# Performance work log

Measured on AMD Instinct MI355X. Metric: run time of the kernel, lower is better.

## Reference

```python
import jax, jax.numpy as jnp
import numpy as np

SMOOTH = 1.0
P = 2
NUM_ITERS = 200  # kornia connected_components num_iterations


def _maxpool3x3(x):
    # F.max_pool2d(x, kernel_size=3, stride=1, padding=1) equivalent (NCHW)
    return jax.lax.reduce_window(
        x, -jnp.inf, jax.lax.max,
        window_dimensions=(1, 1, 3, 3),
        window_strides=(1, 1, 1, 1),
        padding='SAME',
    )


def connected_components(mask_f, num_iterations=NUM_ITERS):
    # kornia-style iterative label propagation on a (B,1,H,W) binary mask.
    # labels initialized to unique pixel ids where mask==1, 0 elsewhere,
    # then 3x3 max-pool propagated, keeping background pinned at 0.
    B, C, H, W = mask_f.shape
    mask = mask_f > 0
    init = jnp.arange(B * C * H * W, dtype=mask_f.dtype).reshape(B, C, H, W)
    out = jnp.where(mask, init, 0.0)

    def body(i, o):
        return jnp.where(mask, _maxpool3x3(o), 0.0)

    return jax.lax.fori_loop(0, num_iterations, body, out)


def setup_inputs() -> dict:
    key = jax.random.key(0)
    k1, k2 = jax.random.split(key)
    B, H, W = 16, 512, 512
    predict = jax.random.uniform(k1, (B, 1, H, W), dtype=jnp.float32)
    target = jax.random.uniform(k2, (B, 1, H, W), dtype=jnp.float32)
    return {"predict": predict, "target": target}


def reference(predict, target):
    B = predict.shape[0]
    # threshold at half of global max -> binary mask (non-differentiable)
    binmask = (predict > (predict.max() / 2)).astype(predict.dtype)
    labels = connected_components(jax.lax.stop_gradient(binmask))

    # torch.numel(torch.unique(labels)) via sort + adjacent-diff count (jit-safe)
    s = jnp.sort(labels.reshape(-1))
    n_unique = 1 + jnp.sum(s[1:] != s[:-1])

    penalty = n_unique.astype(jnp.float32) / B
    penalty = jnp.where(penalty < 1.0, jnp.float32(B), penalty)
    penalty = jnp.minimum(penalty, jnp.float32(B))

    p = predict.reshape(B, -1)
    t = target.reshape(B, -1)
    num = jnp.sum(p * t, axis=1) + SMOOTH
    den = jnp.sum(p ** P + t ** P, axis=1) + SMOOTH
    loss = 1.0 - num / den
    return loss.mean() * penalty  # reduction='mean'
```

## Files before the change

### kernel.cpp

```cpp
#include <hip/hip_runtime.h>
#include <hip/hip_cooperative_groups.h>
#include <stdint.h>

namespace cg = cooperative_groups;

#define NPIX   (16 * 512 * 512)
#define IMG    (512 * 512)
#define NB     16

#define CORE   64
#define HALO   8
#define KIT    8
#define NROUND 25
#define TW     88
#define TH     82
#define TX0    4

#define BM_WORDS  (NPIX / 32)
#define NREP      16
#define SAT       256u
#define MAX3(a, b, c) max(max((a), (b)), (c))

__global__ __launch_bounds__(256) void k_maxdice(const float4* __restrict__ pr4,
                                                 const float4* __restrict__ tg4,
                                                 unsigned int* __restrict__ umax,
                                                 float* __restrict__ num,
                                                 float* __restrict__ den) {
    unsigned int m = 0;
    float sn = 0.f, sd = 0.f;
    int base = blockIdx.x * 1024;
#pragma unroll
    for (int k = 0; k < 4; ++k) {
        int i4 = base + k * 256 + threadIdx.x;
        float4 p = pr4[i4], t = tg4[i4];
        m = max(m, __float_as_uint(p.x));
        m = max(m, __float_as_uint(p.y));
        m = max(m, __float_as_uint(p.z));
        m = max(m, __float_as_uint(p.w));
        sn += p.x * t.x + p.y * t.y + p.z * t.z + p.w * t.w;
        sd += p.x * p.x + p.y * p.y + p.z * p.z + p.w * p.w
            + t.x * t.x + t.y * t.y + t.z * t.z + t.w * t.w;
    }
    for (int o = 32; o > 0; o >>= 1) {
        m  = max(m, (unsigned int)__shfl_down(m, o, 64));
        sn += __shfl_down(sn, o, 64);
        sd += __shfl_down(sd, o, 64);
    }
    __shared__ unsigned int sm[4];
    __shared__ float wn[4], wd[4];
    int lane = threadIdx.x & 63, w = threadIdx.x >> 6;
    if (lane == 0) { sm[w] = m; wn[w] = sn; wd[w] = sd; }
    __syncthreads();
    if (threadIdx.x == 0) {
        atomicMax(umax, max(max(sm[0], sm[1]), max(sm[2], sm[3])));
        int b = blockIdx.x >> 6;
        atomicAdd(&num[b * 32], wn[0] + wn[1] + wn[2] + wn[3]);
        atomicAdd(&den[b * 32], wd[0] + wd[1] + wd[2] + wd[3]);
    }
}

__global__ __launch_bounds__(256) void k_iso(const float* __restrict__ pr,
                                             const unsigned int* __restrict__ umax,
                                             unsigned int* __restrict__ isoCnt) {
    const float thr = __uint_as_float(*umax) * 0.5f;
    unsigned int cnt = 0;
    const int tid = threadIdx.x;
    for (int k = 0; k < 8; ++k) {
        int i4 = (blockIdx.x * 8 + k) * 256 + tid;
        int px = i4 * 4;
        int y   = (px >> 9) & 511;
        int gxr = px & 511;
        float4 c = *(const float4*)(pr + px);
        bool m0 = c.x > thr, m1 = c.y > thr, m2 = c.z > thr, m3 = c.w > thr;
        bool lc = (gxr > 0)   && pr[px - 1] > thr;
        bool rc = (gxr < 508) && pr[px + 4] > thr;
        bool u0 = false, u1 = false, u2 = false, u3 = false, lu = false, ru = false;
        if (y > 0) {
            float4 u = *(const float4*)(pr + px - 512);
            u0 = u.x > thr; u1 = u.y > thr; u2 = u.z > thr; u3 = u.w > thr;
            lu = (gxr > 0)   && pr[px - 513] > thr;
            ru = (gxr < 508) && pr[px - 508] > thr;
        }
        bool d0 = false, d1 = false, d2 = false, d3 = false, ld = false, rd = false;
        if (y < 511) {
            float4 d = *(const float4*)(pr + px + 512);
            d0 = d.x > thr; d1 = d.y > thr; d2 = d.z > thr; d3 = d.w > thr;
            ld = (gxr > 0)   && pr[px + 511] > thr;
            rd = (gxr < 508) && pr[px + 516] > thr;
        }
        bool v0 = u0 | d0, v1 = u1 | d1, v2 = u2 | d2, v3 = u3 | d3;
        bool cmL = lu | lc | ld, cmR = ru | rc | rd;
        bool cm0 = v0 | m0, cm1 = v1 | m1, cm2 = v2 | m2, cm3 = v3 | m3;
        cnt += (m0 && !(cmL | cm1 | v0) && px > 0) ? 1u : 0u;
        cnt += (m1 && !(cm0 | cm2 | v1)) ? 1u : 0u;
        cnt += (m2 && !(cm1 | cm3 | v2)) ? 1u : 0u;
        cnt += (m3 && !(cm2 | cmR | v3)) ? 1u : 0u;
    }
    for (int o = 32; o > 0; o >>= 1)
        cnt += __shfl_down(cnt, o, 64);
    __shared__ unsigned int sc[4];
    int lane = tid & 63, w = tid >> 6;
    if (lane == 0) sc[w] = cnt;
    __syncthreads();
    if (tid == 0)
        atomicAdd(isoCnt, sc[0] + sc[1] + sc[2] + sc[3]);
}

__global__ __launch_bounds__(256, 4) void k_prop_all(const float* __restrict__ pr,
                                                     int* __restrict__ bufA,
                                                     int* __restrict__ bufB,
                                                     unsigned int* __restrict__ bm,
                                                     const unsigned int* __restrict__ umax,
                                                     const unsigned int* __restrict__ isoCnt) {
    if (*isoCnt >= SAT) return;
    cg::grid_group grid = cg::this_grid();
    __shared__ int T[TH * TW];
    const float thr = __uint_as_float(*umax) * 0.5f;
    const int tid  = threadIdx.x;
    const int blk  = blockIdx.x;
    const int bx   = blk & 7, by = (blk >> 3) & 7, bimg = blk >> 6;
    const int gx0  = bx * CORE - HALO;
    const int gy0  = by * CORE - HALO;
    int* const base0 = bufA + bimg * IMG;
    int* const base1 = bufB + bimg * IMG;
    const float* img = pr + bimg * IMG;

    {
        int4* bmz = (int4*)bm;
        for (int u = blk * 256 + tid; u < NREP * BM_WORDS / 4; u += 1024 * 256)
            bmz[u] = make_int4(0, 0, 0, 0);
    }

    if (tid < TW) { T[tid] = -1; T[81 * TW + tid] = -1; }
    if (tid < 80) { T[(tid + 1) * TW + 3] = -1; T[(tid + 1) * TW + 84] = -1; }
    for (int u = tid; u < 1600; u += 256) {
        int r = u / 20, c = (u % 20) * 4;
        int gy = gy0 + r, gx = gx0 + c;
        int4 v;
        if (gy >= 0 && gy < 512 && gx >= 0 && gx < 512) {
            float4 pv = *(const float4*)(img + (gy << 9) + gx);
            int id = bimg * IMG + (gy << 9) + gx;
            v.x = (pv.x > thr) ? id     : -1;
            v.y = (pv.y > thr) ? id + 1 : -1;
            v.z = (pv.z > thr) ? id + 2 : -1;
            v.w = (pv.w > thr) ? id + 3 : -1;
        } else v = make_int4(-1, -1, -1, -1);
        *(int4*)&T[(r + 1) * TW + TX0 + c] = v;
    }
    __syncthreads();
    grid.sync();

    const bool active = (tid < 200);
    const int cu = tid % 20, ru = tid / 20;
    const int x0 = cu * 4;
    const int yr = ru * 8;
    int4 O[8];

#define LOAD_ROW(y, V, VL, VR) do {                            \
        const int* _r = &T[((y) + 1) * TW + TX0 + x0];         \
        V  = *(const int4*)_r;                                 \
        VL = _r[-1];                                           \
        VR = _r[4];                                            \
    } while (0)

    for (int r = 0; r < NROUND; ++r) {
        for (int it = 0; it < KIT; ++it) {
            if (active) {
                int4 A, B, C; int Al, Ar, Bl, Br, Cl, Cr;
                LOAD_ROW(yr - 1, A, Al, Ar);
                LOAD_ROW(yr,     B, Bl, Br);
#pragma unroll
                for (int j = 0; j < 8; ++j) {
                    LOAD_ROW(yr + j + 1, C, Cl, Cr);
                    int4 col;
                    col.x = MAX3(A.x, B.x, C.x);
                    col.y = MAX3(A.y, B.y, C.y);
                    col.z = MAX3(A.z, B.z, C.z);
                    col.w = MAX3(A.w, B.w, C.w);
                    int cl = MAX3(Al, Bl, Cl);
                    int cr = MAX3(Ar, Br, Cr);
                    O[j].x = MAX3(cl,    col.x, col.y) | (B.x >> 31);
                    O[j].y = MAX3(col.x, col.y, col.z) | (B.y >> 31);
                    O[j].z = MAX3(col.y, col.z, col.w) | (B.z >> 31);
                    O[j].w = MAX3(col.z, col.w, cr)    | (B.w >> 31);
                    A = B; Al = Bl; Ar = Br;
                    B = C; Bl = Cl; Br = Cr;
                }
            }
            __syncthreads();
            if (active) {
#pragma unroll
                for (int j = 0; j < 8; ++j)
                    *(int4*)&T[(yr + j + 1) * TW + TX0 + x0] = O[j];
            }
            __syncthreads();
        }

        if (r < NROUND - 1) {
            int* dst = (r & 1) ? base1 : base0;
            for (int u = tid; u < 448; u += 256) {
                int lr, lc;
                if (u < 128)      { lr = u >> 4;                lc = u & 15; }
                else if (u < 256) { lr = 56 + ((u - 128) >> 4); lc = u & 15; }
                else { int v = u - 256; lr = 8 + (v >> 2); int s = v & 3; lc = (s < 2) ? s : 12 + s; }
                int4 val = *(const int4*)&T[(HALO + lr + 1) * TW + TX0 + HALO + lc * 4];
                *(int4*)(dst + ((by * CORE + lr) << 9) + bx * CORE + lc * 4) = val;
            }
            __threadfence();
            grid.sync();
            const int* src = (r & 1) ? base1 : base0;
            for (int u = tid; u < 576; u += 256) {
                int lrow, lcu;
                if (u < 160)      { lrow = u / 20;              lcu = u % 20; }
                else if (u < 320) { lrow = 72 + (u - 160) / 20; lcu = u % 20; }
                else { int v = u - 320; lrow = 8 + (v >> 2); int s = v & 3; lcu = (s < 2) ? s : 16 + s; }
                int gy = gy0 + lrow, gx = gx0 + lcu * 4;
                int4 val = (gy >= 0 && gy < 512 && gx >= 0 && gx < 512)
                           ? *(const int4*)(src + (gy << 9) + gx)
                           : make_int4(-1, -1, -1, -1);
                *(int4*)&T[(lrow + 1) * TW + TX0 + lcu * 4] = val;
            }
            __syncthreads();
        } else {
            for (int u = tid; u < 1024; u += 256) {
                int lr = u >> 4, lc = u & 15;
                int4 val = *(const int4*)&T[(HALO + lr + 1) * TW + TX0 + HALO + lc * 4];
                *(int4*)(base0 + ((by * CORE + lr) << 9) + bx * CORE + lc * 4) = val;
            }
        }
    }
#undef LOAD_ROW
}

__global__ __launch_bounds__(256) void k_bits(const int* __restrict__ lab,
                                              unsigned int* __restrict__ bm,
                                              const unsigned int* __restrict__ isoCnt) {
    if (*isoCnt >= SAT) return;
    __shared__ unsigned int sk[1024];
    __shared__ int slot[256];
    const int tid = threadIdx.x;
    unsigned int* rep = bm + (blockIdx.x & (NREP - 1)) * BM_WORDS;
    for (int k = 0; k < 4; ++k) {
        if (k) __syncthreads();
        const int i4 = blockIdx.x * 1024 + k * 256 + tid;
        int4 c = ((const int4*)lab)[i4];
        int pw = __shfl_up(c.w, 1, 64);
        unsigned int prevk;
        if ((tid & 63) == 0) {
            if (i4 == 0) prevk = ~0u;
            else { int pv = lab[i4 * 4 - 1]; prevk = (pv < 0) ? 0u : (unsigned int)pv; }
        } else {
            prevk = (pw < 0) ? 0u : (unsigned int)pw;
        }
        unsigned int k0 = (c.x < 0) ? 0u : (unsigned int)c.x;
        unsigned int k1 = (c.y < 0) ? 0u : (unsigned int)c.y;
        unsigned int k2 = (c.z < 0) ? 0u : (unsigned int)c.z;
        unsigned int k3 = (c.w < 0) ? 0u : (unsigned int)c.w;
        bool c0 = (k0 != prevk), c1 = (k1 != k0), c2 = (k2 != k1), c3 = (k3 != k2);
        sk[0 * 256 + tid] = k0;
        sk[1 * 256 + tid] = k1;
        sk[2 * 256 + tid] = k2;
        sk[3 * 256 + tid] = k3;
        if (c0) slot[k0 & 255] = tid * 4 + 0;
        if (c1) slot[k1 & 255] = tid * 4 + 1;
        if (c2) slot[k2 & 255] = tid * 4 + 2;
        if (c3) slot[k3 & 255] = tid * 4 + 3;
        __syncthreads();
#define SKAT(w) sk[((w) & 3) * 256 + ((w) >> 2)]
        if (c0) { int w = slot[k0 & 255]; if (w != tid * 4 + 0 && SKAT(w) == k0) c0 = false; }
        if (c1) { int w = slot[k1 & 255]; if (w != tid * 4 + 1 && SKAT(w) == k1) c1 = false; }
        if (c2) { int w = slot[k2 & 255]; if (w != tid * 4 + 2 && SKAT(w) == k2) c2 = false; }
        if (c3) { int w = slot[k3 & 255]; if (w != tid * 4 + 3 && SKAT(w) == k3) c3 = false; }
#undef SKAT
#define TSET(kk, cc) if (cc) {                                        \
            unsigned int word = rep[(kk) >> 5];                       \
            if (!((word >> ((kk) & 31)) & 1u))                        \
                atomicOr(&rep[(kk) >> 5], 1u << ((kk) & 31));         \
        }
        TSET(k0, c0); TSET(k1, c1); TSET(k2, c2); TSET(k3, c3);
#undef TSET
    }
}

__global__ void k_popc(const unsigned int* __restrict__ bm, unsigned int* nuniq, int words,
                       const unsigned int* __restrict__ isoCnt) {
    if (*isoCnt >= SAT) return;
    unsigned int c = 0;
    for (int i = blockIdx.x * blockDim.x + threadIdx.x; i < words; i += gridDim.x * blockDim.x) {
        unsigned int w = 0;
#pragma unroll
        for (int r = 0; r < NREP; ++r) w |= bm[r * BM_WORDS + i];
        c += __popc(w);
    }
    for (int o = 32; o > 0; o >>= 1)
        c += __shfl_down(c, o, 64);
    __shared__ unsigned int sc[4];
    int lane = threadIdx.x & 63, w = threadIdx.x >> 6;
    if (lane == 0) sc[w] = c;
    __syncthreads();
    if (threadIdx.x == 0)
        atomicAdd(nuniq, sc[0] + sc[1] + sc[2] + sc[3]);
}

__global__ void k_final(const unsigned int* __restrict__ nuniq,
                        const unsigned int* __restrict__ isoCnt,
                        const float* __restrict__ num, const float* __restrict__ den,
                        float* __restrict__ out) {
    float loss = 0.0f;
    for (int b = 0; b < NB; ++b)
        loss += 1.0f - (num[b * 32] + 1.0f) / (den[b * 32] + 1.0f);
    loss *= (1.0f / NB);
    float penalty;
    if (*isoCnt >= SAT) {
        penalty = (float)NB;
    } else {
        penalty = (float)(*nuniq) / (float)NB;
        if (penalty < 1.0f) penalty = (float)NB;
        penalty = fminf(penalty, (float)NB);
    }
    out[0] = loss * penalty;
}

extern "C" void kernel_launch(void* const* d_in, const int* in_sizes, int n_in,
                              void* d_out, int out_size, void* d_ws, size_t ws_size,
                              hipStream_t stream) {
    const float* predict = (const float*)d_in[0];
    const float* target  = (const float*)d_in[1];
    float* out = (float*)d_out;

    char* ws = (char*)d_ws;
    unsigned int* umax   = (unsigned int*)ws;
    unsigned int* nuniq  = (unsigned int*)(ws + 4);
    unsigned int* isoCnt = (unsigned int*)(ws + 8);
    float* num = (float*)(ws + 256);
    float* den = (float*)(ws + 2304);
    int* labA = (int*)(ws + 16384);
    int* labB = labA + NPIX;
    unsigned int* bm = (unsigned int*)(ws + 16384 + (size_t)2 * NPIX * sizeof(int));

    hipMemsetAsync(ws, 0, 8192, stream);

    k_maxdice<<<1024, 256, 0, stream>>>((const float4*)predict, (const float4*)target,
                                        umax, num, den);
    k_iso<<<512, 256, 0, stream>>>(predict, umax, isoCnt);

    void* args[] = { (void*)&predict, (void*)&labA, (void*)&labB,
                     (void*)&bm, (void*)&umax, (void*)&isoCnt };
    hipLaunchCooperativeKernel((void*)k_prop_all, dim3(1024), dim3(256), args, 0, stream);

    k_bits<<<NPIX / 4096, 256, 0, stream>>>(labA, bm, isoCnt);
    k_popc<<<512, 256, 0, stream>>>(bm, nuniq, BM_WORDS, isoCnt);
    k_final<<<1, 1, 0, stream>>>(nuniq, isoCnt, num, den, out);
}
```

Baseline: 141.2 us.

## Fold bitmap and popcount stages into cooperative kernel and drop global atomics

Per-block max, dice partial sums and isolated-pixel counts are now written to per-block arrays and reduced inside the consumer kernels, so the atomics and the workspace memset are no longer needed. The bitmap-marking and popcount kernels are merged into the cooperative propagation kernel behind extra grid syncs. The final kernel becomes a 256-thread reduction. The aim is fewer launches and less serialized atomic traffic, at the cost of every block redundantly re-reducing the 1024 or 512 partials and of two more grid-wide barriers when propagation runs.

```diff
diff --git a/kernel.cpp b/kernel.cpp
--- a/kernel.cpp
+++ b/kernel.cpp
@@ -23,9 +23,9 @@
 
 __global__ __launch_bounds__(256) void k_maxdice(const float4* __restrict__ pr4,
                                                  const float4* __restrict__ tg4,
-                                                 unsigned int* __restrict__ umax,
-                                                 float* __restrict__ num,
-                                                 float* __restrict__ den) {
+                                                 unsigned int* __restrict__ umaxArr,
+                                                 float* __restrict__ numArr,
+                                                 float* __restrict__ denArr) {
     unsigned int m = 0;
     float sn = 0.f, sd = 0.f;
     int base = blockIdx.x * 1024;
@@ -52,17 +52,47 @@
     if (lane == 0) { sm[w] = m; wn[w] = sn; wd[w] = sd; }
     __syncthreads();
     if (threadIdx.x == 0) {
-        atomicMax(umax, max(max(sm[0], sm[1]), max(sm[2], sm[3])));
-        int b = blockIdx.x >> 6;
-        atomicAdd(&num[b * 32], wn[0] + wn[1] + wn[2] + wn[3]);
-        atomicAdd(&den[b * 32], wd[0] + wd[1] + wd[2] + wd[3]);
-    }
+        umaxArr[blockIdx.x] = max(max(sm[0], sm[1]), max(sm[2], sm[3]));
+        numArr[blockIdx.x]  = wn[0] + wn[1] + wn[2] + wn[3];
+        denArr[blockIdx.x]  = wd[0] + wd[1] + wd[2] + wd[3];
+    }
+}
+
+__device__ float block_thr(const unsigned int* __restrict__ umaxArr) {
+    const int tid = threadIdx.x;
+    unsigned int m = max(max(umaxArr[tid], umaxArr[tid + 256]),
+                         max(umaxArr[tid + 512], umaxArr[tid + 768]));
+    for (int o = 32; o > 0; o >>= 1)
+        m = max(m, (unsigned int)__shfl_down(m, o, 64));
+    __shared__ unsigned int sm[4];
+    __shared__ unsigned int smax;
+    int lane = tid & 63, w = tid >> 6;
+    if (lane == 0) sm[w] = m;
+    __syncthreads();
+    if (tid == 0) smax = max(max(sm[0], sm[1]), max(sm[2], sm[3]));
+    __syncthreads();
+    return __uint_as_float(smax) * 0.5f;
+}
+
+__device__ unsigned int block_iso(const unsigned int* __restrict__ isoArr) {
+    const int tid = threadIdx.x;
+    unsigned int c = isoArr[tid] + isoArr[tid + 256];
+    for (int o = 32; o > 0; o >>= 1)
+        c += __shfl_down(c, o, 64);
+    __shared__ unsigned int sc[4];
+    __shared__ unsigned int stot;
+    int lane = tid & 63, w = tid >> 6;
+    if (lane == 0) sc[w] = c;
+    __syncthreads();
+    if (tid == 0) stot = sc[0] + sc[1] + sc[2] + sc[3];
+    __syncthreads();
+    return stot;
 }
 
 __global__ __launch_bounds__(256) void k_iso(const float* __restrict__ pr,
-                                             const unsigned int* __restrict__ umax,
-                                             unsigned int* __restrict__ isoCnt) {
-    const float thr = __uint_as_float(*umax) * 0.5f;
+                                             const unsigned int* __restrict__ umaxArr,
+                                             unsigned int* __restrict__ isoArr) {
+    const float thr = block_thr(umaxArr);
     unsigned int cnt = 0;
     const int tid = threadIdx.x;
     for (int k = 0; k < 8; ++k) {
@@ -103,19 +133,20 @@
     if (lane == 0) sc[w] = cnt;
     __syncthreads();
     if (tid == 0)
-        atomicAdd(isoCnt, sc[0] + sc[1] + sc[2] + sc[3]);
+        isoArr[blockIdx.x] = sc[0] + sc[1] + sc[2] + sc[3];
 }
 
 __global__ __launch_bounds__(256, 4) void k_prop_all(const float* __restrict__ pr,
                                                      int* __restrict__ bufA,
                                                      int* __restrict__ bufB,
                                                      unsigned int* __restrict__ bm,
-                                                     const unsigned int* __restrict__ umax,
-                                                     const unsigned int* __restrict__ isoCnt) {
-    if (*isoCnt >= SAT) return;
+                                                     const unsigned int* __restrict__ umaxArr,
+                                                     const unsigned int* __restrict__ isoArr,
+                                                     unsigned int* __restrict__ nuniq) {
+    if (block_iso(isoArr) >= SAT) return;
     cg::grid_group grid = cg::this_grid();
     __shared__ int T[TH * TW];
-    const float thr = __uint_as_float(*umax) * 0.5f;
+    const float thr = block_thr(umaxArr);
     const int tid  = threadIdx.x;
     const int blk  = blockIdx.x;
     const int bx   = blk & 7, by = (blk >> 3) & 7, bimg = blk >> 6;
@@ -125,6 +156,7 @@
     int* const base1 = bufB + bimg * IMG;
     const float* img = pr + bimg * IMG;
 
+    if (blk == 0 && tid == 0) *nuniq = 0;
     {
         int4* bmz = (int4*)bm;
         for (int u = blk * 256 + tid; u < NREP * BM_WORDS / 4; u += 1024 * 256)
@@ -230,95 +262,116 @@
         }
     }
 #undef LOAD_ROW
-}
-
-__global__ __launch_bounds__(256) void k_bits(const int* __restrict__ lab,
-                                              unsigned int* __restrict__ bm,
-                                              const unsigned int* __restrict__ isoCnt) {
-    if (*isoCnt >= SAT) return;
-    __shared__ unsigned int sk[1024];
-    __shared__ int slot[256];
-    const int tid = threadIdx.x;
-    unsigned int* rep = bm + (blockIdx.x & (NREP - 1)) * BM_WORDS;
-    for (int k = 0; k < 4; ++k) {
-        if (k) __syncthreads();
-        const int i4 = blockIdx.x * 1024 + k * 256 + tid;
-        int4 c = ((const int4*)lab)[i4];
-        int pw = __shfl_up(c.w, 1, 64);
-        unsigned int prevk;
-        if ((tid & 63) == 0) {
-            if (i4 == 0) prevk = ~0u;
-            else { int pv = lab[i4 * 4 - 1]; prevk = (pv < 0) ? 0u : (unsigned int)pv; }
-        } else {
-            prevk = (pw < 0) ? 0u : (unsigned int)pw;
-        }
-        unsigned int k0 = (c.x < 0) ? 0u : (unsigned int)c.x;
-        unsigned int k1 = (c.y < 0) ? 0u : (unsigned int)c.y;
-        unsigned int k2 = (c.z < 0) ? 0u : (unsigned int)c.z;
-        unsigned int k3 = (c.w < 0) ? 0u : (unsigned int)c.w;
-        bool c0 = (k0 != prevk), c1 = (k1 != k0), c2 = (k2 != k1), c3 = (k3 != k2);
-        sk[0 * 256 + tid] = k0;
-        sk[1 * 256 + tid] = k1;
-        sk[2 * 256 + tid] = k2;
-        sk[3 * 256 + tid] = k3;
-        if (c0) slot[k0 & 255] = tid * 4 + 0;
-        if (c1) slot[k1 & 255] = tid * 4 + 1;
-        if (c2) slot[k2 & 255] = tid * 4 + 2;
-        if (c3) slot[k3 & 255] = tid * 4 + 3;
-        __syncthreads();
+
+    __threadfence();
+    grid.sync();
+    {
+        const int* lab = bufA;
+        __shared__ unsigned int sk[1024];
+        __shared__ int slot[256];
+        unsigned int* rep = bm + (blk & (NREP - 1)) * BM_WORDS;
+        for (int k = 0; k < 4; ++k) {
+            __syncthreads();
+            const int i4 = blk * 1024 + k * 256 + tid;
+            int4 c = ((const int4*)lab)[i4];
+            int pw = __shfl_up(c.w, 1, 64);
+            unsigned int prevk;
+            if ((tid & 63) == 0) {
+                if (i4 == 0) prevk = ~0u;
+                else { int pv = lab[i4 * 4 - 1]; prevk = (pv < 0) ? 0u : (unsigned int)pv; }
+            } else {
+                prevk = (pw < 0) ? 0u : (unsigned int)pw;
+            }
+            unsigned int k0 = (c.x < 0) ? 0u : (unsigned int)c.x;
+            unsigned int k1 = (c.y < 0) ? 0u : (unsigned int)c.y;
+            unsigned int k2 = (c.z < 0) ? 0u : (unsigned int)c.z;
+            unsigned int k3 = (c.w < 0) ? 0u : (unsigned int)c.w;
+            bool c0 = (k0 != prevk), c1 = (k1 != k0), c2 = (k2 != k1), c3 = (k3 != k2);
+            sk[0 * 256 + tid] = k0;
+            sk[1 * 256 + tid] = k1;
+            sk[2 * 256 + tid] = k2;
+            sk[3 * 256 + tid] = k3;
+            if (c0) slot[k0 & 255] = tid * 4 + 0;
+            if (c1) slot[k1 & 255] = tid * 4 + 1;
+            if (c2) slot[k2 & 255] = tid * 4 + 2;
+            if (c3) slot[k3 & 255] = tid * 4 + 3;
+            __syncthreads();
 #define SKAT(w) sk[((w) & 3) * 256 + ((w) >> 2)]
-        if (c0) { int w = slot[k0 & 255]; if (w != tid * 4 + 0 && SKAT(w) == k0) c0 = false; }
-        if (c1) { int w = slot[k1 & 255]; if (w != tid * 4 + 1 && SKAT(w) == k1) c1 = false; }
-        if (c2) { int w = slot[k2 & 255]; if (w != tid * 4 + 2 && SKAT(w) == k2) c2 = false; }
-        if (c3) { int w = slot[k3 & 255]; if (w != tid * 4 + 3 && SKAT(w) == k3) c3 = false; }
+            if (c0) { int w = slot[k0 & 255]; if (w != tid * 4 + 0 && SKAT(w) == k0) c0 = false; }
+            if (c1) { int w = slot[k1 & 255]; if (w != tid * 4 + 1 && SKAT(w) == k1) c1 = false; }
+            if (c2) { int w = slot[k2 & 255]; if (w != tid * 4 + 2 && SKAT(w) == k2) c2 = false; }
+            if (c3) { int w = slot[k3 & 255]; if (w != tid * 4 + 3 && SKAT(w) == k3) c3 = false; }
 #undef SKAT
 #define TSET(kk, cc) if (cc) {                                        \
-            unsigned int word = rep[(kk) >> 5];                       \
-            if (!((word >> ((kk) & 31)) & 1u))                        \
-                atomicOr(&rep[(kk) >> 5], 1u << ((kk) & 31));         \
-        }
-        TSET(k0, c0); TSET(k1, c1); TSET(k2, c2); TSET(k3, c3);
+                unsigned int word = rep[(kk) >> 5];                   \
+                if (!((word >> ((kk) & 31)) & 1u))                    \
+                    atomicOr(&rep[(kk) >> 5], 1u << ((kk) & 31));     \
+            }
+            TSET(k0, c0); TSET(k1, c1); TSET(k2, c2); TSET(k3, c3);
 #undef TSET
-    }
-}
-
-__global__ void k_popc(const unsigned int* __restrict__ bm, unsigned int* nuniq, int words,
-                       const unsigned int* __restrict__ isoCnt) {
-    if (*isoCnt >= SAT) return;
-    unsigned int c = 0;
-    for (int i = blockIdx.x * blockDim.x + threadIdx.x; i < words; i += gridDim.x * blockDim.x) {
-        unsigned int w = 0;
+        }
+    }
+
+    __threadfence();
+    grid.sync();
+    {
+        unsigned int c = 0;
+        for (int i = blk * 256 + tid; i < BM_WORDS; i += 1024 * 256) {
+            unsigned int w = 0;
 #pragma unroll
-        for (int r = 0; r < NREP; ++r) w |= bm[r * BM_WORDS + i];
-        c += __popc(w);
-    }
-    for (int o = 32; o > 0; o >>= 1)
-        c += __shfl_down(c, o, 64);
-    __shared__ unsigned int sc[4];
-    int lane = threadIdx.x & 63, w = threadIdx.x >> 6;
-    if (lane == 0) sc[w] = c;
-    __syncthreads();
-    if (threadIdx.x == 0)
-        atomicAdd(nuniq, sc[0] + sc[1] + sc[2] + sc[3]);
-}
-
-__global__ void k_final(const unsigned int* __restrict__ nuniq,
-                        const unsigned int* __restrict__ isoCnt,
-                        const float* __restrict__ num, const float* __restrict__ den,
-                        float* __restrict__ out) {
-    float loss = 0.0f;
-    for (int b = 0; b < NB; ++b)
-        loss += 1.0f - (num[b * 32] + 1.0f) / (den[b * 32] + 1.0f);
-    loss *= (1.0f / NB);
-    float penalty;
-    if (*isoCnt >= SAT) {
-        penalty = (float)NB;
-    } else {
-        penalty = (float)(*nuniq) / (float)NB;
-        if (penalty < 1.0f) penalty = (float)NB;
-        penalty = fminf(penalty, (float)NB);
-    }
-    out[0] = loss * penalty;
+            for (int r = 0; r < NREP; ++r) w |= bm[r * BM_WORDS + i];
+            c += __popc(w);
+        }
+        for (int o = 32; o > 0; o >>= 1)
+            c += __shfl_down(c, o, 64);
+        __shared__ unsigned int pc[4];
+        int lane = tid & 63, w = tid >> 6;
+        if (lane == 0) pc[w] = c;
+        __syncthreads();
+        if (tid == 0 && (pc[0] | pc[1] | pc[2] | pc[3]))
+            atomicAdd(nuniq, pc[0] + pc[1] + pc[2] + pc[3]);
+    }
+}
+
+__global__ __launch_bounds__(256) void k_final(const unsigned int* __restrict__ isoArr,
+                                               const unsigned int* __restrict__ nuniq,
+                                               const float* __restrict__ numArr,
+                                               const float* __restrict__ denArr,
+                                               float* __restrict__ out) {
+    const int tid = threadIdx.x;
+    unsigned int isoSum = block_iso(isoArr);
+
+    __shared__ float rn[256], rd[256], lossArr[16];
+    int b = tid >> 4, l = tid & 15;
+    float sn = 0.f, sd = 0.f;
+#pragma unroll
+    for (int k = 0; k < 4; ++k) {
+        int s = b * 64 + l + 16 * k;
+        sn += numArr[s];
+        sd += denArr[s];
+    }
+    rn[tid] = sn; rd[tid] = sd;
+    __syncthreads();
+    if (l == 0) {
+        float tn = 0.f, td = 0.f;
+        for (int j = 0; j < 16; ++j) { tn += rn[tid + j]; td += rd[tid + j]; }
+        lossArr[b] = 1.0f - (tn + 1.0f) / (td + 1.0f);
+    }
+    __syncthreads();
+    if (tid == 0) {
+        float loss = 0.f;
+        for (int j = 0; j < 16; ++j) loss += lossArr[j];
+        loss *= (1.0f / NB);
+        float penalty;
+        if (isoSum >= SAT) {
+            penalty = (float)NB;
+        } else {
+            penalty = (float)(*nuniq) / (float)NB;
+            if (penalty < 1.0f) penalty = (float)NB;
+            penalty = fminf(penalty, (float)NB);
+        }
+        out[0] = loss * penalty;
+    }
 }
 
 extern "C" void kernel_launch(void* const* d_in, const int* in_sizes, int n_in,
@@ -329,26 +382,22 @@
     float* out = (float*)d_out;
 
     char* ws = (char*)d_ws;
-    unsigned int* umax   = (unsigned int*)ws;
-    unsigned int* nuniq  = (unsigned int*)(ws + 4);
-    unsigned int* isoCnt = (unsigned int*)(ws + 8);
-    float* num = (float*)(ws + 256);
-    float* den = (float*)(ws + 2304);
+    unsigned int* umaxArr = (unsigned int*)ws;
+    float* numArr = (float*)(ws + 4096);
+    float* denArr = (float*)(ws + 8192);
+    unsigned int* isoArr = (unsigned int*)(ws + 12288);
+    unsigned int* nuniq  = (unsigned int*)(ws + 14336);
     int* labA = (int*)(ws + 16384);
     int* labB = labA + NPIX;
     unsigned int* bm = (unsigned int*)(ws + 16384 + (size_t)2 * NPIX * sizeof(int));
 
-    hipMemsetAsync(ws, 0, 8192, stream);
-
     k_maxdice<<<1024, 256, 0, stream>>>((const float4*)predict, (const float4*)target,
-                                        umax, num, den);
-    k_iso<<<512, 256, 0, stream>>>(predict, umax, isoCnt);
+                                        umaxArr, numArr, denArr);
+    k_iso<<<512, 256, 0, stream>>>(predict, umaxArr, isoArr);
 
     void* args[] = { (void*)&predict, (void*)&labA, (void*)&labB,
-                     (void*)&bm, (void*)&umax, (void*)&isoCnt };
+                     (void*)&bm, (void*)&umaxArr, (void*)&isoArr, (void*)&nuniq };
     hipLaunchCooperativeKernel((void*)k_prop_all, dim3(1024), dim3(256), args, 0, stream);
 
-    k_bits<<<NPIX / 4096, 256, 0, stream>>>(labA, bm, isoCnt);
-    k_popc<<<512, 256, 0, stream>>>(bm, nuniq, BM_WORDS, isoCnt);
-    k_final<<<1, 1, 0, stream>>>(nuniq, isoCnt, num, den, out);
-}
+    k_final<<<1, 256, 0, stream>>>(isoArr, nuniq, numArr, denArr, out);
+}
```

Result: faster. 119.5 us (-15.3%).
